# Kernel tuning notes

Hardware: AMD Instinct MI355X
Metric: run time of the kernel (lower is better)

The kernel has to match this reference:

```python
import jax, jax.numpy as jnp
import numpy as np

N_HEAD = 16
MASK_VALUE = -10000.0


def setup_inputs() -> dict:
    key = jax.random.key(0)
    k1, k2, k3 = jax.random.split(key, 3)
    B, S, D = 2, 2048, 1024
    x = jax.random.normal(k1, (B, S, D), dtype=jnp.float32)
    W_qkv = jax.random.normal(k2, (D, 3 * D), dtype=jnp.float32) * 0.02
    b_qkv = jnp.zeros((3 * D,), dtype=jnp.float32)
    W_out = jax.random.normal(k3, (D, D), dtype=jnp.float32) * 0.02
    b_out = jnp.zeros((D,), dtype=jnp.float32)
    return {"x": x, "W_qkv": W_qkv, "b_qkv": b_qkv, "W_out": W_out, "b_out": b_out}


def reference(x, W_qkv, b_qkv, W_out, b_out):
    B, S, D = x.shape
    H = N_HEAD
    hd = D // H
    # fused QKV projection
    qkv = x @ W_qkv + b_qkv                      # [B, S, 3D]
    q, k, v = jnp.split(qkv, 3, axis=-1)
    # split heads -> [B, H, S, hd]
    def split_heads(t):
        return t.reshape(B, S, H, hd).transpose(0, 2, 1, 3)
    q, k, v = split_heads(q), split_heads(k), split_heads(v)
    # scaled causal attention with explicit mask-fill (matches ops.attention)
    scale = 1.0 / jnp.sqrt(jnp.asarray(hd, dtype=x.dtype))
    w = jnp.einsum('bhqd,bhkd->bhqk', q, k) * scale   # [B, H, S, S]
    causal = jnp.tril(jnp.ones((S, S), dtype=bool))    # [S, S]
    w = jnp.where(causal, w, jnp.asarray(MASK_VALUE, dtype=w.dtype))
    a = jax.nn.softmax(w, axis=-1)
    o = jnp.einsum('bhqk,bhkd->bhqd', a, v)            # [B, H, S, hd]
    # merge heads -> [B, S, D]
    o = o.transpose(0, 2, 1, 3).reshape(B, S, D)
    out = o @ W_out + b_out
    return out
```

## Files before the change

### kernel.cpp

```cpp
#include <hip/hip_runtime.h>
#include <hip/hip_bf16.h>
#include <stdint.h>

#define BATCH 2
#define SEQ   2048
#define DIM   1024
#define NH    16
#define HD    64
#define MVAL  (-10000.0f)

typedef __attribute__((ext_vector_type(8))) short bf16x8;
typedef __attribute__((ext_vector_type(4))) float f32x4;
typedef unsigned short u16;

static __device__ __forceinline__ u16 f2bf(float f) {
  union { float f; uint32_t u; } c; c.f = f;
  uint32_t x = c.u;
  return (u16)((x + 0x7fffu + ((x >> 16) & 1u)) >> 16);
}

static __device__ __forceinline__ uint32_t pk2(float a, float b) {
  __hip_bfloat162 h = __float22bfloat162_rn(make_float2(a, b));
  union { __hip_bfloat162 h; uint32_t u; } c; c.h = h;
  return c.u;
}

static __device__ __forceinline__ int swz128(int row, int chunk) {
  return row * 128 + (((chunk ^ (row & 7)) & 7) << 4);
}

static __device__ __forceinline__ void gload_lds16(const void* g, void* l) {
  __builtin_amdgcn_global_load_lds((const __attribute__((address_space(1))) void*)g,
                                   (__attribute__((address_space(3))) void*)l, 16, 0, 0);
}

__global__ void cvt_kernel(const float* __restrict__ in, u16* __restrict__ out, int n4) {
  int i = blockIdx.x * blockDim.x + threadIdx.x;
  if (i < n4) {
    float4 v = reinterpret_cast<const float4*>(in)[i];
    reinterpret_cast<uint2*>(out)[i] = make_uint2(pk2(v.x, v.y), pk2(v.z, v.w));
  }
}

__global__ void transpose_cvt_kernel(const float* __restrict__ in, u16* __restrict__ out,
                                     int R, int C) {
  __shared__ float tile[32][33];
  int c0 = blockIdx.x * 32, r0 = blockIdx.y * 32;
  int tx = threadIdx.x, ty = threadIdx.y;
#pragma unroll
  for (int i = 0; i < 32; i += 8)
    tile[ty + i][tx] = in[(size_t)(r0 + ty + i) * C + c0 + tx];
  __syncthreads();
#pragma unroll
  for (int i = 0; i < 32; i += 8)
    out[(size_t)(c0 + ty + i) * R + r0 + tx] = f2bf(tile[tx][ty + i]);
}

__global__ void vtrans_kernel(const u16* __restrict__ Vi, u16* __restrict__ Vo) {
  __shared__ __align__(16) char t[8192];
  int tid = threadIdx.x;
  int bh = blockIdx.y, s0 = blockIdx.x * 64;
  const u16* src = Vi + ((size_t)bh * SEQ + s0) * HD;
#pragma unroll
  for (int i = 0; i < 2; i++) {
    int r = i * 32 + (tid >> 3), ch = tid & 7;
    uint4 v = *reinterpret_cast<const uint4*>(src + (size_t)r * HD + ch * 8);
    *reinterpret_cast<uint4*>(t + swz128(r, ch)) = v;
  }
  __syncthreads();
  int d = tid >> 2, sc = tid & 3;
  u16 vals[16];
#pragma unroll
  for (int j = 0; j < 16; j++) {
    int s = sc * 16 + j;
    vals[j] = *reinterpret_cast<const u16*>(
        t + s * 128 + ((((d >> 3) ^ (s & 7)) & 7) << 4) + (d & 7) * 2);
  }
  u16* dst = Vo + ((size_t)bh * HD + d) * SEQ + s0 + sc * 16;
  *reinterpret_cast<uint4*>(dst) = *reinterpret_cast<const uint4*>(vals);
  *reinterpret_cast<uint4*>(dst + 8) = *reinterpret_cast<const uint4*>(vals + 8);
}

template <int EPI>
__global__ __launch_bounds__(256, 2) void gemm_bt_kernel(
    const u16* __restrict__ A, const u16* __restrict__ Bt,
    const float* __restrict__ bias, float* __restrict__ Cout,
    u16* __restrict__ Qo, u16* __restrict__ Ko, u16* __restrict__ Vo,
    int M, int N, int K) {
  __shared__ __align__(16) char lds[32768];
  char* As = lds;
  char* Bs = lds + 16384;
  int tid = threadIdx.x;
  int lane = tid & 63, l15 = lane & 15, l4 = lane >> 4;
  int w = tid >> 6, wr = w >> 1, wc = w & 1;
  int m0 = blockIdx.y * 128, n0 = blockIdx.x * 128;
  int srow = tid >> 3, sch = tid & 7;
  int sc_swz = ((sch ^ (srow & 7)) << 3);

  const u16* Ap = A + (size_t)(m0 + srow) * K + sc_swz;
  const u16* Bp = Bt + (size_t)(n0 + srow) * K + sc_swz;

  f32x4 acc[4][4] = {};

  for (int k0 = 0; k0 < K; k0 += 64) {
    __syncthreads();
#pragma unroll
    for (int i = 0; i < 4; i++) {
      gload_lds16(Ap + (size_t)i * 32 * K + k0, As + i * 4096 + tid * 16);
      gload_lds16(Bp + (size_t)i * 32 * K + k0, Bs + i * 4096 + tid * 16);
    }
    __syncthreads();
#pragma unroll
    for (int ks = 0; ks < 2; ks++) {
      int ch = ks * 4 + l4;
      bf16x8 af[4], bfv[4];
#pragma unroll
      for (int mi = 0; mi < 4; mi++)
        af[mi] = *reinterpret_cast<const bf16x8*>(As + swz128(wr * 64 + mi * 16 + l15, ch));
#pragma unroll
      for (int nj = 0; nj < 4; nj++)
        bfv[nj] = *reinterpret_cast<const bf16x8*>(Bs + swz128(wc * 64 + nj * 16 + l15, ch));
#pragma unroll
      for (int nj = 0; nj < 4; nj++)
#pragma unroll
        for (int mi = 0; mi < 4; mi++)
          acc[nj][mi] = __builtin_amdgcn_mfma_f32_16x16x32_bf16(bfv[nj], af[mi], acc[nj][mi], 0, 0, 0);
    }
  }

#pragma unroll
  for (int nj = 0; nj < 4; nj++) {
    int nb = n0 + wc * 64 + nj * 16 + l4 * 4;
    float4 bv = *reinterpret_cast<const float4*>(bias + nb);
#pragma unroll
    for (int mi = 0; mi < 4; mi++) {
      int m = m0 + wr * 64 + mi * 16 + l15;
      f32x4 a = acc[nj][mi];
      float v0 = a[0] + bv.x, v1 = a[1] + bv.y, v2 = a[2] + bv.z, v3 = a[3] + bv.w;
      if (EPI == 1) {
        *reinterpret_cast<float4*>(Cout + (size_t)m * N + nb) = make_float4(v0, v1, v2, v3);
      } else {
        int b = m >> 11, s = m & 2047;
        int sec = nb >> 10, c = nb & 1023, h = c >> 6, d = c & 63;
        size_t bh = (size_t)(b * NH + h);
        u16* dst;
        float scl;
        if (sec == 0)      { dst = Qo; scl = 0.125f; }
        else if (sec == 1) { dst = Ko; scl = 1.0f; }
        else               { dst = Vo; scl = 1.0f; }
        *reinterpret_cast<uint2*>(dst + (bh * SEQ + s) * HD + d) =
            make_uint2(pk2(v0 * scl, v1 * scl), pk2(v2 * scl, v3 * scl));
      }
    }
  }
}

__global__ __launch_bounds__(256, 2) void attn_kernel(
    const u16* __restrict__ Q, const u16* __restrict__ K,
    const u16* __restrict__ Vt, u16* __restrict__ O) {
  __shared__ __align__(16) char lds[81920];
  int tid = threadIdx.x, lane = tid & 63, w = tid >> 6;
  int l15 = lane & 15, l4 = lane >> 4;
  int sub = w & 1, par = w >> 1;
  int blk = blockIdx.x;
  int bh = (blk & 7) * 4 + ((blk >> 3) & 3);
  int p = blk >> 5;
  const u16* Qh = Q + (size_t)bh * SEQ * HD;
  const u16* Kh = K + (size_t)bh * SEQ * HD;
  const u16* Vh = Vt + (size_t)bh * HD * SEQ;
  char* Pw = lds + 65536 + w * 4096;
  int srow = tid >> 3, sch = tid & 7;
  int b_ = bh >> 4, h_ = bh & 15;

  auto stageKV = [&](int b, int T) {
    const u16* Kt = Kh + (size_t)T * 128 * HD;
    const u16* Vs = Vh + (size_t)T * 128;
    char* Kb = lds + b * 16384;
    char* Vb = lds + 32768 + b * 16384;
#pragma unroll
    for (int i = 0; i < 4; i++) {
      int row = i * 32 + srow;
      int c = (sch ^ (row & 7)) << 3;
      gload_lds16(Kt + (size_t)row * HD + c, Kb + row * 128 + sch * 16);
    }
#pragma unroll
    for (int sv = 0; sv < 2; sv++)
#pragma unroll
      for (int i = 0; i < 2; i++) {
        int d = i * 32 + srow;
        int c = (sch ^ (d & 7)) << 3;
        gload_lds16(Vs + (size_t)d * SEQ + sv * 64 + c, Vb + sv * 8192 + d * 128 + sch * 16);
      }
  };

  int buf = 0;
  stageKV(0, 0);
  __syncthreads();

  for (int pass = 0; pass < 2; pass++) {
    int qt = (pass == 0) ? (31 - p) : p;
    int nT = (qt + 2) >> 1;
    int qb = qt * 64 + sub * 32;

    bf16x8 qf[2][2];
#pragma unroll
    for (int mi = 0; mi < 2; mi++)
#pragma unroll
      for (int ks = 0; ks < 2; ks++)
        qf[mi][ks] = *reinterpret_cast<const bf16x8*>(
            Qh + (size_t)(qb + mi * 16 + l15) * HD + ks * 32 + l4 * 8);

    float mrun[2] = {-1e30f, -1e30f}, lrun[2] = {0.0f, 0.0f};
    f32x4 oacc[4][2] = {};

    for (int T = 0; T < nT; T++) {
      int nxt = (T + 1 < nT) ? (T + 1) : (pass == 0 ? 0 : -1);
      if (nxt >= 0) stageKV(buf ^ 1, nxt);

      char* Kw = lds + buf * 16384 + par * 8192;
      char* Vw = lds + 32768 + buf * 16384 + par * 8192;
      int kvb = T * 128 + par * 64;

      f32x4 s[4][2] = {};
      __builtin_amdgcn_s_setprio(1);
#pragma unroll
      for (int ks = 0; ks < 2; ks++)
#pragma unroll
        for (int nj = 0; nj < 4; nj++) {
          bf16x8 kf = *reinterpret_cast<const bf16x8*>(Kw + swz128(nj * 16 + l15, ks * 4 + l4));
#pragma unroll
          for (int mi = 0; mi < 2; mi++)
            s[nj][mi] = __builtin_amdgcn_mfma_f32_16x16x32_bf16(kf, qf[mi][ks], s[nj][mi], 0, 0, 0);
        }
      __builtin_amdgcn_s_setprio(0);

      if (kvb + 63 > qb) {
#pragma unroll
        for (int nj = 0; nj < 4; nj++)
#pragma unroll
          for (int mi = 0; mi < 2; mi++) {
            int qg = qb + mi * 16 + l15;
#pragma unroll
            for (int r = 0; r < 4; r++) {
              int kg = kvb + nj * 16 + l4 * 4 + r;
              if (kg > qg) s[nj][mi][r] = MVAL;
            }
          }
      }

      float alpha[2];
#pragma unroll
      for (int mi = 0; mi < 2; mi++) {
        float mt = s[0][mi][0];
#pragma unroll
        for (int nj = 0; nj < 4; nj++)
#pragma unroll
          for (int r = 0; r < 4; r++) mt = fmaxf(mt, s[nj][mi][r]);
        mt = fmaxf(mt, __shfl_xor(mt, 16));
        mt = fmaxf(mt, __shfl_xor(mt, 32));
        float mnew = fmaxf(mrun[mi], mt);
        alpha[mi] = __expf(mrun[mi] - mnew);
        mrun[mi] = mnew;
        float rs = 0.0f;
        int prow = mi * 16 + l15;
#pragma unroll
        for (int nj = 0; nj < 4; nj++) {
          float p0 = __expf(s[nj][mi][0] - mnew);
          float p1 = __expf(s[nj][mi][1] - mnew);
          float p2 = __expf(s[nj][mi][2] - mnew);
          float p3 = __expf(s[nj][mi][3] - mnew);
          rs += (p0 + p1) + (p2 + p3);
          int chunk = nj * 2 + (l4 >> 1);
          char* dst = Pw + prow * 128 + (((chunk ^ (prow & 7)) & 7) << 4) + (l4 & 1) * 8;
          *reinterpret_cast<uint2*>(dst) = make_uint2(pk2(p0, p1), pk2(p2, p3));
        }
        rs += __shfl_xor(rs, 16);
        rs += __shfl_xor(rs, 32);
        lrun[mi] = lrun[mi] * alpha[mi] + rs;
      }
#pragma unroll
      for (int nd = 0; nd < 4; nd++)
#pragma unroll
        for (int mi = 0; mi < 2; mi++)
#pragma unroll
          for (int r = 0; r < 4; r++) oacc[nd][mi][r] *= alpha[mi];

      asm volatile("s_waitcnt lgkmcnt(0)" ::: "memory");
      __builtin_amdgcn_sched_barrier(0);

      bf16x8 pf[2][2];
#pragma unroll
      for (int mi = 0; mi < 2; mi++)
#pragma unroll
        for (int ks = 0; ks < 2; ks++)
          pf[mi][ks] = *reinterpret_cast<const bf16x8*>(Pw + swz128(mi * 16 + l15, ks * 4 + l4));

      __builtin_amdgcn_s_setprio(1);
#pragma unroll
      for (int ks = 0; ks < 2; ks++)
#pragma unroll
        for (int nd = 0; nd < 4; nd++) {
          bf16x8 vf = *reinterpret_cast<const bf16x8*>(Vw + swz128(nd * 16 + l15, ks * 4 + l4));
#pragma unroll
          for (int mi = 0; mi < 2; mi++)
            oacc[nd][mi] = __builtin_amdgcn_mfma_f32_16x16x32_bf16(vf, pf[mi][ks], oacc[nd][mi], 0, 0, 0);
        }
      __builtin_amdgcn_s_setprio(0);

      __syncthreads();
      buf ^= 1;
    }

    char* Xo = lds + (buf ^ 1) * 16384;
    float* Xml = (float*)(lds + 65536);
    if (par == 1) {
#pragma unroll
      for (int mi = 0; mi < 2; mi++) {
        int row = sub * 32 + mi * 16 + l15;
        if (l4 == 0) {
          Xml[row * 2] = mrun[mi];
          Xml[row * 2 + 1] = lrun[mi];
        }
#pragma unroll
        for (int nd = 0; nd < 4; nd++)
          *reinterpret_cast<f32x4*>(Xo + row * 256 + (((nd * 4 + l4) ^ (row & 7)) << 4)) =
              oacc[nd][mi];
      }
    }
    __syncthreads();
    if (par == 0) {
#pragma unroll
      for (int mi = 0; mi < 2; mi++) {
        int row = sub * 32 + mi * 16 + l15;
        float mB = Xml[row * 2], lB = Xml[row * 2 + 1];
        float m = fmaxf(mrun[mi], mB);
        float wA = __expf(mrun[mi] - m), wB = __expf(mB - m);
        float linv = 1.0f / (lrun[mi] * wA + lB * wB);
        u16* orow = O + ((size_t)b_ * SEQ + qt * 64 + sub * 32 + mi * 16 + l15) * DIM + h_ * HD;
#pragma unroll
        for (int nd = 0; nd < 4; nd++) {
          f32x4 ob = *reinterpret_cast<const f32x4*>(
              Xo + row * 256 + (((nd * 4 + l4) ^ (row & 7)) << 4));
          float o0 = (oacc[nd][mi][0] * wA + ob[0] * wB) * linv;
          float o1 = (oacc[nd][mi][1] * wA + ob[1] * wB) * linv;
          float o2 = (oacc[nd][mi][2] * wA + ob[2] * wB) * linv;
          float o3 = (oacc[nd][mi][3] * wA + ob[3] * wB) * linv;
          *reinterpret_cast<uint2*>(orow + nd * 16 + l4 * 4) = make_uint2(pk2(o0, o1), pk2(o2, o3));
        }
      }
    }
    __syncthreads();
  }
}

extern "C" void kernel_launch(void* const* d_in, const int* in_sizes, int n_in,
                              void* d_out, int out_size, void* d_ws, size_t ws_size,
                              hipStream_t stream) {
  const float* x     = (const float*)d_in[0];
  const float* W_qkv = (const float*)d_in[1];
  const float* b_qkv = (const float*)d_in[2];
  const float* W_out = (const float*)d_in[3];
  const float* b_out = (const float*)d_in[4];
  float* out = (float*)d_out;
  char* ws = (char*)d_ws;

  u16* xb    = (u16*)(ws);
  u16* WqkvT = (u16*)(ws + 8388608);
  u16* WoutT = (u16*)(ws + 8388608 + 6291456);
  u16* Qb    = (u16*)(ws + 16777216);
  u16* Kb    = (u16*)(ws + 16777216 + 8388608);
  u16* Vtb   = (u16*)(ws + 16777216 + 2 * 8388608);
  u16* Ob    = (u16*)(ws + 16777216 + 3 * 8388608);
  u16* Vraw  = Ob;

  cvt_kernel<<<4096, 256, 0, stream>>>(x, xb, BATCH * SEQ * DIM / 4);
  transpose_cvt_kernel<<<dim3(3 * DIM / 32, DIM / 32), dim3(32, 8), 0, stream>>>(
      W_qkv, WqkvT, DIM, 3 * DIM);
  transpose_cvt_kernel<<<dim3(DIM / 32, DIM / 32), dim3(32, 8), 0, stream>>>(
      W_out, WoutT, DIM, DIM);
  gemm_bt_kernel<0><<<dim3(3 * DIM / 128, BATCH * SEQ / 128), 256, 0, stream>>>(
      xb, WqkvT, b_qkv, nullptr, Qb, Kb, Vraw, BATCH * SEQ, 3 * DIM, DIM);
  vtrans_kernel<<<dim3(SEQ / 64, BATCH * NH), 256, 0, stream>>>(Vraw, Vtb);
  attn_kernel<<<512, 256, 0, stream>>>(Qb, Kb, Vtb, Ob);
  gemm_bt_kernel<1><<<dim3(DIM / 128, BATCH * SEQ / 128), 256, 0, stream>>>(
      Ob, WoutT, b_out, out, nullptr, nullptr, nullptr, BATCH * SEQ, DIM, DIM);
}
```

Measured before the change: 127.0 us.

## Fold log2e into Q scale, compute row sums via MFMA, skip unneeded rescales

```diff
diff --git a/kernel.cpp b/kernel.cpp
--- a/kernel.cpp
+++ b/kernel.cpp
@@ -145,7 +145,7 @@
         size_t bh = (size_t)(b * NH + h);
         u16* dst;
         float scl;
-        if (sec == 0)      { dst = Qo; scl = 0.125f; }
+        if (sec == 0)      { dst = Qo; scl = 0.125f * 1.44269504f; }
         else if (sec == 1) { dst = Ko; scl = 1.0f; }
         else               { dst = Vo; scl = 1.0f; }
         *reinterpret_cast<uint2*>(dst + (bh * SEQ + s) * HD + d) =
@@ -172,6 +172,10 @@
   int srow = tid >> 3, sch = tid & 7;
   int b_ = bh >> 4, h_ = bh & 15;
 
+  bf16x8 onesf;
+#pragma unroll
+  for (int j = 0; j < 8; j++) onesf[j] = (short)0x3F80;
+
   auto stageKV = [&](int b, int T) {
     const u16* Kt = Kh + (size_t)T * 128 * HD;
     const u16* Vs = Vh + (size_t)T * 128;
@@ -210,8 +214,9 @@
         qf[mi][ks] = *reinterpret_cast<const bf16x8*>(
             Qh + (size_t)(qb + mi * 16 + l15) * HD + ks * 32 + l4 * 8);
 
-    float mrun[2] = {-1e30f, -1e30f}, lrun[2] = {0.0f, 0.0f};
+    float mrun[2] = {-1e30f, -1e30f};
     f32x4 oacc[4][2] = {};
+    f32x4 acc_l[2] = {};
 
     for (int T = 0; T < nT; T++) {
       int nxt = (T + 1 < nT) ? (T + 1) : (pass == 0 ? 0 : -1);
@@ -233,6 +238,13 @@
             s[nj][mi] = __builtin_amdgcn_mfma_f32_16x16x32_bf16(kf, qf[mi][ks], s[nj][mi], 0, 0, 0);
         }
       __builtin_amdgcn_s_setprio(0);
+
+      bf16x8 vf[4][2];
+#pragma unroll
+      for (int ks = 0; ks < 2; ks++)
+#pragma unroll
+        for (int nd = 0; nd < 4; nd++)
+          vf[nd][ks] = *reinterpret_cast<const bf16x8*>(Vw + swz128(nd * 16 + l15, ks * 4 + l4));
 
       if (kvb + 63 > qb) {
 #pragma unroll
@@ -248,42 +260,48 @@
           }
       }
 
-      float alpha[2];
+      float mt[2];
 #pragma unroll
       for (int mi = 0; mi < 2; mi++) {
-        float mt = s[0][mi][0];
+        float m = s[0][mi][0];
 #pragma unroll
         for (int nj = 0; nj < 4; nj++)
 #pragma unroll
-          for (int r = 0; r < 4; r++) mt = fmaxf(mt, s[nj][mi][r]);
-        mt = fmaxf(mt, __shfl_xor(mt, 16));
-        mt = fmaxf(mt, __shfl_xor(mt, 32));
-        float mnew = fmaxf(mrun[mi], mt);
-        alpha[mi] = __expf(mrun[mi] - mnew);
-        mrun[mi] = mnew;
-        float rs = 0.0f;
+          for (int r = 0; r < 4; r++) m = fmaxf(m, s[nj][mi][r]);
+        m = fmaxf(m, __shfl_xor(m, 16));
+        m = fmaxf(m, __shfl_xor(m, 32));
+        mt[mi] = m;
+      }
+
+      if (!__all((mt[0] <= mrun[0]) & (mt[1] <= mrun[1]))) {
+#pragma unroll
+        for (int mi = 0; mi < 2; mi++) {
+          float mnew = fmaxf(mrun[mi], mt[mi]);
+          float alpha = exp2f(mrun[mi] - mnew);
+          mrun[mi] = mnew;
+#pragma unroll
+          for (int nd = 0; nd < 4; nd++)
+#pragma unroll
+            for (int r = 0; r < 4; r++) oacc[nd][mi][r] *= alpha;
+#pragma unroll
+          for (int r = 0; r < 4; r++) acc_l[mi][r] *= alpha;
+        }
+      }
+
+#pragma unroll
+      for (int mi = 0; mi < 2; mi++) {
         int prow = mi * 16 + l15;
 #pragma unroll
         for (int nj = 0; nj < 4; nj++) {
-          float p0 = __expf(s[nj][mi][0] - mnew);
-          float p1 = __expf(s[nj][mi][1] - mnew);
-          float p2 = __expf(s[nj][mi][2] - mnew);
-          float p3 = __expf(s[nj][mi][3] - mnew);
-          rs += (p0 + p1) + (p2 + p3);
+          float p0 = exp2f(s[nj][mi][0] - mrun[mi]);
+          float p1 = exp2f(s[nj][mi][1] - mrun[mi]);
+          float p2 = exp2f(s[nj][mi][2] - mrun[mi]);
+          float p3 = exp2f(s[nj][mi][3] - mrun[mi]);
           int chunk = nj * 2 + (l4 >> 1);
           char* dst = Pw + prow * 128 + (((chunk ^ (prow & 7)) & 7) << 4) + (l4 & 1) * 8;
           *reinterpret_cast<uint2*>(dst) = make_uint2(pk2(p0, p1), pk2(p2, p3));
         }
-        rs += __shfl_xor(rs, 16);
-        rs += __shfl_xor(rs, 32);
-        lrun[mi] = lrun[mi] * alpha[mi] + rs;
-      }
-#pragma unroll
-      for (int nd = 0; nd < 4; nd++)
-#pragma unroll
-        for (int mi = 0; mi < 2; mi++)
-#pragma unroll
-          for (int r = 0; r < 4; r++) oacc[nd][mi][r] *= alpha[mi];
+      }
 
       asm volatile("s_waitcnt lgkmcnt(0)" ::: "memory");
       __builtin_amdgcn_sched_barrier(0);
@@ -297,14 +315,16 @@
 
       __builtin_amdgcn_s_setprio(1);
 #pragma unroll
-      for (int ks = 0; ks < 2; ks++)
-#pragma unroll
-        for (int nd = 0; nd < 4; nd++) {
-          bf16x8 vf = *reinterpret_cast<const bf16x8*>(Vw + swz128(nd * 16 + l15, ks * 4 + l4));
+      for (int ks = 0; ks < 2; ks++) {
+#pragma unroll
+        for (int nd = 0; nd < 4; nd++)
 #pragma unroll
           for (int mi = 0; mi < 2; mi++)
-            oacc[nd][mi] = __builtin_amdgcn_mfma_f32_16x16x32_bf16(vf, pf[mi][ks], oacc[nd][mi], 0, 0, 0);
-        }
+            oacc[nd][mi] = __builtin_amdgcn_mfma_f32_16x16x32_bf16(vf[nd][ks], pf[mi][ks], oacc[nd][mi], 0, 0, 0);
+#pragma unroll
+        for (int mi = 0; mi < 2; mi++)
+          acc_l[mi] = __builtin_amdgcn_mfma_f32_16x16x32_bf16(onesf, pf[mi][ks], acc_l[mi], 0, 0, 0);
+      }
       __builtin_amdgcn_s_setprio(0);
 
       __syncthreads();
@@ -319,7 +339,7 @@
         int row = sub * 32 + mi * 16 + l15;
         if (l4 == 0) {
           Xml[row * 2] = mrun[mi];
-          Xml[row * 2 + 1] = lrun[mi];
+          Xml[row * 2 + 1] = acc_l[mi][0];
         }
 #pragma unroll
         for (int nd = 0; nd < 4; nd++)
@@ -334,17 +354,18 @@
         int row = sub * 32 + mi * 16 + l15;
         float mB = Xml[row * 2], lB = Xml[row * 2 + 1];
         float m = fmaxf(mrun[mi], mB);
-        float wA = __expf(mrun[mi] - m), wB = __expf(mB - m);
-        float linv = 1.0f / (lrun[mi] * wA + lB * wB);
+        float wA = exp2f(mrun[mi] - m), wB = exp2f(mB - m);
+        float linv = 1.0f / (acc_l[mi][0] * wA + lB * wB);
+        float fA = wA * linv, fB = wB * linv;
         u16* orow = O + ((size_t)b_ * SEQ + qt * 64 + sub * 32 + mi * 16 + l15) * DIM + h_ * HD;
 #pragma unroll
         for (int nd = 0; nd < 4; nd++) {
           f32x4 ob = *reinterpret_cast<const f32x4*>(
               Xo + row * 256 + (((nd * 4 + l4) ^ (row & 7)) << 4));
-          float o0 = (oacc[nd][mi][0] * wA + ob[0] * wB) * linv;
-          float o1 = (oacc[nd][mi][1] * wA + ob[1] * wB) * linv;
-          float o2 = (oacc[nd][mi][2] * wA + ob[2] * wB) * linv;
-          float o3 = (oacc[nd][mi][3] * wA + ob[3] * wB) * linv;
+          float o0 = oacc[nd][mi][0] * fA + ob[0] * fB;
+          float o1 = oacc[nd][mi][1] * fA + ob[1] * fB;
+          float o2 = oacc[nd][mi][2] * fA + ob[2] * fB;
+          float o3 = oacc[nd][mi][3] * fA + ob[3] * fB;
           *reinterpret_cast<uint2*>(orow + nd * 16 + l4 * 4) = make_uint2(pk2(o0, o1), pk2(o2, o3));
         }
       }
```

Result: slower. 133.6 us (+5.2%).
